# Kernel tuning notes

Hardware: AMD Instinct MI355X
Metric: run time of the kernel (lower is better)

Reference implementation:

```python
import jax, jax.numpy as jnp
import numpy as np

B, N, D = 8, 4096, 1024
NC, NU = 8, 32            # core / universal experts (num_experts=16, occ_factor=1/4)
E = NC + NU               # 40 total experts
S = 2                     # slots per expert
HC, HU = 4 * D, D         # core hidden = 4*dim, occ hidden = 4*occ_factor*dim = dim
L2_EPS = 1e-6
LN_EPS = 1e-5


def l2norm(x):
    n = jnp.sqrt(jnp.sum(x * x, axis=-1, keepdims=True))
    return x * (1.0 / (n + L2_EPS))


def layernorm(x, g, b):
    mu = jnp.mean(x, axis=-1, keepdims=True)
    var = jnp.mean((x - mu) ** 2, axis=-1, keepdims=True)
    return (x - mu) / jnp.sqrt(var + LN_EPS) * g + b


def entmax15(z):
    # exact 1.5-entmax over last axis (sorted algorithm, Peters et al. 2019)
    z = z / 2.0
    z = z - jnp.max(z, axis=-1, keepdims=True)
    zs = -jnp.sort(-z, axis=-1)                      # descending
    K = z.shape[-1]
    k = jnp.arange(1, K + 1, dtype=z.dtype)
    mean = jnp.cumsum(zs, axis=-1) / k
    meansq = jnp.cumsum(zs * zs, axis=-1) / k
    ss = k * (meansq - mean * mean)
    delta = jnp.maximum((1.0 - ss) / k, 1e-12)
    tau = mean - jnp.sqrt(delta)
    support = jnp.sum((tau <= zs).astype(jnp.int32), axis=-1, keepdims=True)
    tau_star = jnp.take_along_axis(tau, support - 1, axis=-1)
    return jnp.maximum(z - tau_star, 0.0) ** 2


def setup_inputs() -> dict:
    key = jax.random.key(0)
    ks = jax.random.split(key, 8)
    return {
        "x": jax.random.normal(ks[0], (B, N, D), jnp.float32),
        "attn_weight": jax.random.uniform(ks[1], (B, 128), jnp.float32),
        "phi": jax.random.normal(ks[2], (E, S, D), jnp.float32) * 0.02,
        "key_gamma": jnp.ones((D,), jnp.float32),
        "key_beta": jnp.zeros((D,), jnp.float32),
        "query_gamma": jnp.ones((D,), jnp.float32),
        "query_beta": jnp.zeros((D,), jnp.float32),
        "ln_gamma": jnp.ones((D,), jnp.float32),
        "ln_beta": jnp.zeros((D,), jnp.float32),
        "scale0": jnp.asarray(0.5, jnp.float32),
        "scale1": jnp.asarray(0.5, jnp.float32),
        "core_w1": jax.random.normal(ks[3], (NC, D, HC), jnp.float32) * (D ** -0.5),
        "core_b1": jnp.zeros((NC, HC), jnp.float32),
        "core_w2": jax.random.normal(ks[4], (NC, HC, D), jnp.float32) * (HC ** -0.5),
        "core_b2": jnp.zeros((NC, D), jnp.float32),
        "occ_w1": jax.random.normal(ks[5], (NU, D, HU), jnp.float32) * (D ** -0.5),
        "occ_b1": jnp.zeros((NU, HU), jnp.float32),
        "occ_w2": jax.random.normal(ks[6], (NU, HU, D), jnp.float32) * (HU ** -0.5),
        "occ_b2": jnp.zeros((NU, D), jnp.float32),
    }


def _expert_mlp(s, w1, b1, w2, b2):
    # s: [b, e, s, d]; per-expert 2-layer MLP with exact GELU
    h = jax.nn.gelu(jnp.einsum('besd,edh->besh', s, w1) + b1[None, :, None, :], approximate=False)
    return jnp.einsum('besh,ehd->besd', h, w2) + b2[None, :, None, :]


def reference(x, attn_weight, phi, key_gamma, key_beta, query_gamma, query_beta,
              ln_gamma, ln_beta, scale0, scale1,
              core_w1, core_b1, core_w2, core_b2,
              occ_w1, occ_b1, occ_w2, occ_b2):
    # keys: OffsetScale then l2norm
    k = l2norm(x * key_gamma + key_beta)
    # queries: OffsetScale -> LayerNorm -> l2norm on phi
    q = layernorm(phi * query_gamma + query_beta, ln_gamma, ln_beta)
    q = l2norm(q)
    logits = jnp.einsum('bnd,esd->bnes', k, q)                      # [B,N,E,S]
    core_mask = (jnp.arange(E) < NC)[None, None, :, None]
    adjusted = jnp.where(core_mask, logits, jnp.asarray(-10000.0, logits.dtype))
    dispatch = jax.nn.softmax(adjusted / scale0, axis=2)            # softmax over experts
    combine = entmax15((adjusted / scale1).reshape(B, N, E * S))    # [B,N,E*S]
    slots = jnp.einsum('bnd,bnes->besd', x, dispatch)               # [B,E,S,D]
    core_out = _expert_mlp(slots[:, :NC], core_w1, core_b1, core_w2, core_b2)
    occ_out = _expert_mlp(slots[:, NC:], occ_w1, occ_b1, occ_w2, occ_b2)
    out = jnp.concatenate([core_out, occ_out], axis=1).reshape(B, E * S, D)
    return jnp.einsum('bsd,bns->bnd', out, combine)                 # [B,N,D]
```

## Files before the change

kernel.cpp:

```cpp
#include <hip/hip_runtime.h>
#include <hip/hip_bf16.h>

#define B_ 8
#define N_ 4096
#define D_ 1024

__global__ __launch_bounds__(64) void k_prep(
    const float* __restrict__ phi, const float* __restrict__ qg, const float* __restrict__ qb,
    const float* __restrict__ lng, const float* __restrict__ lnb,
    const float* __restrict__ kg, const float* __restrict__ kb,
    float* __restrict__ qk, float* __restrict__ cj, float* __restrict__ wbuf)
{
    int r = blockIdx.x;
    int lane = threadIdx.x;
    if (r == 16) {
        float cacc = 0.f;
#pragma unroll
        for (int c = 0; c < 16; ++c) {
            int i = c * 64 + lane;
            float g = kg[i], b = kb[i];
            wbuf[i] = g * g;
            wbuf[1024 + i] = 2.0f * g * b;
            cacc += b * b;
        }
#pragma unroll
        for (int m = 32; m; m >>= 1) cacc += __shfl_xor(cacc, m);
        if (lane == 0) wbuf[2048] = cacc;
        return;
    }
    const float* pr = phi + (size_t)r * D_;
    float v[16];
    float s1 = 0.f;
#pragma unroll
    for (int c = 0; c < 16; ++c) {
        int i = c * 64 + lane;
        v[c] = pr[i] * qg[i] + qb[i];
        s1 += v[c];
    }
#pragma unroll
    for (int m = 32; m; m >>= 1) s1 += __shfl_xor(s1, m);
    float mu = s1 * (1.0f / D_);
    float s2 = 0.f;
#pragma unroll
    for (int c = 0; c < 16; ++c) { float dd = v[c] - mu; s2 += dd * dd; }
#pragma unroll
    for (int m = 32; m; m >>= 1) s2 += __shfl_xor(s2, m);
    float var = s2 * (1.0f / D_);
    float inv = 1.0f / sqrtf(var + 1e-5f);
    float u[16];
    float s3 = 0.f;
#pragma unroll
    for (int c = 0; c < 16; ++c) {
        int i = c * 64 + lane;
        u[c] = (v[c] - mu) * inv * lng[i] + lnb[i];
        s3 += u[c] * u[c];
    }
#pragma unroll
    for (int m = 32; m; m >>= 1) s3 += __shfl_xor(s3, m);
    float rn = 1.0f / (sqrtf(s3) + 1e-6f);
    float cacc = 0.f;
#pragma unroll
    for (int c = 0; c < 16; ++c) {
        int i = c * 64 + lane;
        float qv = u[c] * rn;
        qk[(size_t)r * D_ + i] = qv * kg[i];
        cacc += qv * kb[i];
    }
#pragma unroll
    for (int m = 32; m; m >>= 1) cacc += __shfl_xor(cacc, m);
    if (lane == 0) cj[r] = cacc;
}

__global__ __launch_bounds__(256) void k_logits(
    const float* __restrict__ x, const float* __restrict__ qk,
    const float* __restrict__ wbuf, float* __restrict__ lgbuf)
{
    __shared__ float xs[2][64 * 68];
    __shared__ float qs[2][16 * 64];
    __shared__ float wsd[2][128];

    int tid = threadIdx.x;
    int tok0 = blockIdx.x * 64;
    int tok32 = tid & 31, gg = tid >> 5;
    int sr = tid >> 4, sc = tid & 15;

    float accA[17], accB[17];
#pragma unroll
    for (int v = 0; v < 17; ++v) { accA[v] = 0.f; accB[v] = 0.f; }

    float4 rx[4], rq;
    float rw = 0.f;

    auto STAGE = [&](int dc) {
#pragma unroll
        for (int i = 0; i < 4; ++i)
            rx[i] = *(const float4*)(x + (size_t)(tok0 + sr + 16 * i) * D_ + dc * 64 + sc * 4);
        rq = *(const float4*)(qk + (size_t)sr * D_ + dc * 64 + sc * 4);
        if (tid < 128) rw = wbuf[(size_t)(tid >> 6) * 1024 + dc * 64 + (tid & 63)];
    };
    auto WRITE = [&](int buf) {
#pragma unroll
        for (int i = 0; i < 4; ++i)
            *(float4*)(&xs[buf][(sr + 16 * i) * 68 + sc * 4]) = rx[i];
        ((float4*)qs[buf])[tid] = rq;
        if (tid < 128) wsd[buf][tid] = rw;
    };
    auto COMPUTE = [&](int buf) {
        const float* xpA = &xs[buf][tok32 * 68 + gg * 8];
        const float* xpB = &xs[buf][(32 + tok32) * 68 + gg * 8];
        const float* qp = &qs[buf][gg * 8];
        const float* wp = &wsd[buf][gg * 8];
#pragma unroll
        for (int dl4 = 0; dl4 < 2; ++dl4) {
            float4 xvA = *(const float4*)(xpA + dl4 * 4);
            float4 xvB = *(const float4*)(xpB + dl4 * 4);
            float4 w2v = *(const float4*)(wp + dl4 * 4);
            float4 w1v = *(const float4*)(wp + 64 + dl4 * 4);
            accA[16] += (w2v.x * xvA.x + w1v.x) * xvA.x + (w2v.y * xvA.y + w1v.y) * xvA.y
                      + (w2v.z * xvA.z + w1v.z) * xvA.z + (w2v.w * xvA.w + w1v.w) * xvA.w;
            accB[16] += (w2v.x * xvB.x + w1v.x) * xvB.x + (w2v.y * xvB.y + w1v.y) * xvB.y
                      + (w2v.z * xvB.z + w1v.z) * xvB.z + (w2v.w * xvB.w + w1v.w) * xvB.w;
#pragma unroll
            for (int j = 0; j < 16; ++j) {
                float4 q4 = *(const float4*)(qp + j * 64 + dl4 * 4);
                accA[j] += xvA.x * q4.x + xvA.y * q4.y + xvA.z * q4.z + xvA.w * q4.w;
                accB[j] += xvB.x * q4.x + xvB.y * q4.y + xvB.z * q4.z + xvB.w * q4.w;
            }
        }
    };

    STAGE(0);
    WRITE(0);
    int cur = 0;
#pragma unroll 1
    for (int dc = 0; dc < 16; ++dc) {
        if (dc < 15) STAGE(dc + 1);
        __syncthreads();
        COMPUTE(cur);
        if (dc < 15) WRITE(cur ^ 1);
        cur ^= 1;
    }
    __syncthreads();

    float* red = &xs[0][0];
#pragma unroll
    for (int v = 0; v < 17; ++v) {
        red[(tok32 * 17 + v) * 8 + gg] = accA[v];
        red[((32 + tok32) * 17 + v) * 8 + gg] = accB[v];
    }
    __syncthreads();

#pragma unroll
    for (int it = 0; it < 5; ++it) {
        int idx = tid + it * 256;
        if (idx < 1088) {
            float4 p0 = *(const float4*)(red + idx * 8);
            float4 p1 = *(const float4*)(red + idx * 8 + 4);
            float sum = ((p0.x + p0.y) + (p0.z + p0.w)) + ((p1.x + p1.y) + (p1.z + p1.w));
            int t = idx / 17, v = idx - t * 17;
            lgbuf[(size_t)(tok0 + t) * 20 + v] = sum;
        }
    }
}

__global__ __launch_bounds__(64) void k_epi(
    const float* __restrict__ lgbuf, const float* __restrict__ cj,
    const float* __restrict__ wbuf,
    const float* __restrict__ s0p, const float* __restrict__ s1p,
    float* __restrict__ combine, float* __restrict__ dispatch)
{
    int tok = blockIdx.x * 64 + threadIdx.x;
    const float* lp = lgbuf + (size_t)tok * 20;
    float s[17];
    float4 q0 = *(const float4*)(lp + 0);
    float4 q1 = *(const float4*)(lp + 4);
    float4 q2 = *(const float4*)(lp + 8);
    float4 q3 = *(const float4*)(lp + 12);
    s[0] = q0.x; s[1] = q0.y; s[2] = q0.z; s[3] = q0.w;
    s[4] = q1.x; s[5] = q1.y; s[6] = q1.z; s[7] = q1.w;
    s[8] = q2.x; s[9] = q2.y; s[10] = q2.z; s[11] = q2.w;
    s[12] = q3.x; s[13] = q3.y; s[14] = q3.z; s[15] = q3.w;
    s[16] = lp[16];

    float ss = s[16] + wbuf[2048];
    float rn = 1.0f / (sqrtf(ss) + 1e-6f);
    float inv0 = 1.0f / s0p[0];
    float inv1h = 0.5f / s1p[0];
    float lg[16];
#pragma unroll
    for (int j = 0; j < 16; ++j) lg[j] = (s[j] + cj[j]) * rn;

    float dsp[16];
#pragma unroll
    for (int sl = 0; sl < 2; ++sl) {
        float a[8], m = -1e30f;
#pragma unroll
        for (int ee = 0; ee < 8; ++ee) { a[ee] = lg[2 * ee + sl] * inv0; m = fmaxf(m, a[ee]); }
        float den = 0.f;
#pragma unroll
        for (int ee = 0; ee < 8; ++ee) { a[ee] = expf(a[ee] - m); den += a[ee]; }
        float r = 1.0f / den;
#pragma unroll
        for (int ee = 0; ee < 8; ++ee) dsp[2 * ee + sl] = a[ee] * r;
    }

    float z[16], zmax = -1e30f;
#pragma unroll
    for (int j = 0; j < 16; ++j) { z[j] = lg[j] * inv1h; zmax = fmaxf(zmax, z[j]); }
#pragma unroll
    for (int j = 0; j < 16; ++j) z[j] -= zmax;
    float zsr[16];
#pragma unroll
    for (int j = 0; j < 16; ++j) zsr[j] = z[j];
#pragma unroll
    for (int rr = 0; rr < 16; ++rr) {
#pragma unroll
        for (int jj = (rr & 1); jj + 1 < 16; jj += 2) {
            float aa = zsr[jj], bb = zsr[jj + 1];
            zsr[jj] = fmaxf(aa, bb);
            zsr[jj + 1] = fminf(aa, bb);
        }
    }
    float cs = 0.f, css = 0.f, tau_star = 0.f;
#pragma unroll
    for (int kk = 1; kk <= 16; ++kk) {
        cs += zsr[kk - 1];
        css += zsr[kk - 1] * zsr[kk - 1];
        float fk = (float)kk;
        float mean = cs / fk, msq = css / fk;
        float ssv = fk * (msq - mean * mean);
        float delta = fmaxf((1.0f - ssv) / fk, 1e-12f);
        float tau = mean - sqrtf(delta);
        tau_star = (tau <= zsr[kk - 1]) ? tau : tau_star;
    }
    float4* cw = (float4*)(combine + (size_t)tok * 16);
    float4* dw = (float4*)(dispatch + (size_t)tok * 16);
#pragma unroll
    for (int q4i = 0; q4i < 4; ++q4i) {
        float4 cv, dv;
        float t0 = fmaxf(z[q4i * 4 + 0] - tau_star, 0.f);
        float t1 = fmaxf(z[q4i * 4 + 1] - tau_star, 0.f);
        float t2 = fmaxf(z[q4i * 4 + 2] - tau_star, 0.f);
        float t3 = fmaxf(z[q4i * 4 + 3] - tau_star, 0.f);
        cv.x = t0 * t0; cv.y = t1 * t1; cv.z = t2 * t2; cv.w = t3 * t3;
        dv.x = dsp[q4i * 4 + 0]; dv.y = dsp[q4i * 4 + 1];
        dv.z = dsp[q4i * 4 + 2]; dv.w = dsp[q4i * 4 + 3];
        cw[q4i] = cv;
        dw[q4i] = dv;
    }
}

__global__ __launch_bounds__(256) void k_slots_partial(
    const float* __restrict__ x, const float* __restrict__ dispatch,
    float* __restrict__ partial)
{
    __shared__ float sm[1024];
    int nc = blockIdx.x, b = blockIdx.y;
    int tid = threadIdx.x;
    int n0 = nc * 64;
    ((float4*)sm)[tid] = ((const float4*)(dispatch + ((size_t)b * N_ + n0) * 16))[tid];
    __syncthreads();

    const float* xp = x + ((size_t)b * N_ + n0) * D_ + tid * 4;
    float4 acc[16];
#pragma unroll
    for (int j = 0; j < 16; ++j) { acc[j].x = 0.f; acc[j].y = 0.f; acc[j].z = 0.f; acc[j].w = 0.f; }
#pragma unroll 8
    for (int n = 0; n < 64; ++n) {
        float4 xv = *(const float4*)(xp + (size_t)n * D_);
        const float4* q4 = (const float4*)(sm + n * 16);
        float4 s0 = q4[0], s1 = q4[1], s2 = q4[2], s3 = q4[3];
        acc[0].x  += s0.x * xv.x; acc[0].y  += s0.x * xv.y; acc[0].z  += s0.x * xv.z; acc[0].w  += s0.x * xv.w;
        acc[1].x  += s0.y * xv.x; acc[1].y  += s0.y * xv.y; acc[1].z  += s0.y * xv.z; acc[1].w  += s0.y * xv.w;
        acc[2].x  += s0.z * xv.x; acc[2].y  += s0.z * xv.y; acc[2].z  += s0.z * xv.z; acc[2].w  += s0.z * xv.w;
        acc[3].x  += s0.w * xv.x; acc[3].y  += s0.w * xv.y; acc[3].z  += s0.w * xv.z; acc[3].w  += s0.w * xv.w;
        acc[4].x  += s1.x * xv.x; acc[4].y  += s1.x * xv.y; acc[4].z  += s1.x * xv.z; acc[4].w  += s1.x * xv.w;
        acc[5].x  += s1.y * xv.x; acc[5].y  += s1.y * xv.y; acc[5].z  += s1.y * xv.z; acc[5].w  += s1.y * xv.w;
        acc[6].x  += s1.z * xv.x; acc[6].y  += s1.z * xv.y; acc[6].z  += s1.z * xv.z; acc[6].w  += s1.z * xv.w;
        acc[7].x  += s1.w * xv.x; acc[7].y  += s1.w * xv.y; acc[7].z  += s1.w * xv.z; acc[7].w  += s1.w * xv.w;
        acc[8].x  += s2.x * xv.x; acc[8].y  += s2.x * xv.y; acc[8].z  += s2.x * xv.z; acc[8].w  += s2.x * xv.w;
        acc[9].x  += s2.y * xv.x; acc[9].y  += s2.y * xv.y; acc[9].z  += s2.y * xv.z; acc[9].w  += s2.y * xv.w;
        acc[10].x += s2.z * xv.x; acc[10].y += s2.z * xv.y; acc[10].z += s2.z * xv.z; acc[10].w += s2.z * xv.w;
        acc[11].x += s2.w * xv.x; acc[11].y += s2.w * xv.y; acc[11].z += s2.w * xv.z; acc[11].w += s2.w * xv.w;
        acc[12].x += s3.x * xv.x; acc[12].y += s3.x * xv.y; acc[12].z += s3.x * xv.z; acc[12].w += s3.x * xv.w;
        acc[13].x += s3.y * xv.x; acc[13].y += s3.y * xv.y; acc[13].z += s3.y * xv.z; acc[13].w += s3.y * xv.w;
        acc[14].x += s3.z * xv.x; acc[14].y += s3.z * xv.y; acc[14].z += s3.z * xv.z; acc[14].w += s3.z * xv.w;
        acc[15].x += s3.w * xv.x; acc[15].y += s3.w * xv.y; acc[15].z += s3.w * xv.z; acc[15].w += s3.w * xv.w;
    }
    float* op = partial + (((size_t)b * 64 + nc) * 16) * 1024 + tid * 4;
#pragma unroll
    for (int j = 0; j < 16; ++j)
        *(float4*)(op + (size_t)j * 1024) = acc[j];
}

__global__ __launch_bounds__(256) void k_slots_reduce(
    const float* __restrict__ partial, float* __restrict__ slotsT)
{
    int j = blockIdx.x, b = blockIdx.y;
    int tid = threadIdx.x;
    const float* p = partial + ((size_t)(b * 64) * 16 + j) * 1024 + tid * 4;
    float4 s; s.x = 0.f; s.y = 0.f; s.z = 0.f; s.w = 0.f;
#pragma unroll 8
    for (int nc = 0; nc < 64; ++nc) {
        float4 v = *(const float4*)(p + (size_t)nc * 16384);
        s.x += v.x; s.y += v.y; s.z += v.z; s.w += v.w;
    }
    int e = j >> 1, sl = j & 1;
    int t = b * 2 + sl;
    float* o = slotsT + ((size_t)e * 1024 + tid * 4) * 16 + t;
    o[0] = s.x; o[16] = s.y; o[32] = s.z; o[48] = s.w;
}

__global__ __launch_bounds__(256) void k_mlp1(
    const float* __restrict__ w1, const float* __restrict__ slotsT,
    float* __restrict__ p1)
{
    __shared__ float sm[1024];
    int cc = blockIdx.x, ks = blockIdx.y, e = blockIdx.z;
    int tid = threadIdx.x;
    int k0 = ks * 64;
    int col = cc * 1024 + tid * 4;
    ((float4*)sm)[tid] = ((const float4*)(slotsT + ((size_t)e * 1024 + k0) * 16))[tid];
    __syncthreads();

    const float* wp = w1 + (size_t)e * 1024 * 4096 + (size_t)k0 * 4096 + col;
    float4 acc[16];
#pragma unroll
    for (int t = 0; t < 16; ++t) { acc[t].x = 0.f; acc[t].y = 0.f; acc[t].z = 0.f; acc[t].w = 0.f; }
#pragma unroll 8
    for (int kk = 0; kk < 64; ++kk) {
        float4 w = *(const float4*)(wp + (size_t)kk * 4096);
        const float4* q4 = (const float4*)(sm + kk * 16);
        float4 s0 = q4[0], s1 = q4[1], s2 = q4[2], s3 = q4[3];
        acc[0].x  += s0.x * w.x; acc[0].y  += s0.x * w.y; acc[0].z  += s0.x * w.z; acc[0].w  += s0.x * w.w;
        acc[1].x  += s0.y * w.x; acc[1].y  += s0.y * w.y; acc[1].z  += s0.y * w.z; acc[1].w  += s0.y * w.w;
        acc[2].x  += s0.z * w.x; acc[2].y  += s0.z * w.y; acc[2].z  += s0.z * w.z; acc[2].w  += s0.z * w.w;
        acc[3].x  += s0.w * w.x; acc[3].y  += s0.w * w.y; acc[3].z  += s0.w * w.z; acc[3].w  += s0.w * w.w;
        acc[4].x  += s1.x * w.x; acc[4].y  += s1.x * w.y; acc[4].z  += s1.x * w.z; acc[4].w  += s1.x * w.w;
        acc[5].x  += s1.y * w.x; acc[5].y  += s1.y * w.y; acc[5].z  += s1.y * w.z; acc[5].w  += s1.y * w.w;
        acc[6].x  += s1.z * w.x; acc[6].y  += s1.z * w.y; acc[6].z  += s1.z * w.z; acc[6].w  += s1.z * w.w;
        acc[7].x  += s1.w * w.x; acc[7].y  += s1.w * w.y; acc[7].z  += s1.w * w.z; acc[7].w  += s1.w * w.w;
        acc[8].x  += s2.x * w.x; acc[8].y  += s2.x * w.y; acc[8].z  += s2.x * w.z; acc[8].w  += s2.x * w.w;
        acc[9].x  += s2.y * w.x; acc[9].y  += s2.y * w.y; acc[9].z  += s2.y * w.z; acc[9].w  += s2.y * w.w;
        acc[10].x += s2.z * w.x; acc[10].y += s2.z * w.y; acc[10].z += s2.z * w.z; acc[10].w += s2.z * w.w;
        acc[11].x += s2.w * w.x; acc[11].y += s2.w * w.y; acc[11].z += s2.w * w.z; acc[11].w += s2.w * w.w;
        acc[12].x += s3.x * w.x; acc[12].y += s3.x * w.y; acc[12].z += s3.x * w.z; acc[12].w += s3.x * w.w;
        acc[13].x += s3.y * w.x; acc[13].y += s3.y * w.y; acc[13].z += s3.y * w.z; acc[13].w += s3.y * w.w;
        acc[14].x += s3.z * w.x; acc[14].y += s3.z * w.y; acc[14].z += s3.z * w.z; acc[14].w += s3.z * w.w;
        acc[15].x += s3.w * w.x; acc[15].y += s3.w * w.y; acc[15].z += s3.w * w.z; acc[15].w += s3.w * w.w;
    }
    float av0[16], av1[16], av2[16], av3[16];
#pragma unroll
    for (int t = 0; t < 16; ++t) { av0[t] = acc[t].x; av1[t] = acc[t].y; av2[t] = acc[t].z; av3[t] = acc[t].w; }
    float* op = p1 + (((size_t)ks * 8 + e) * 4096 + col) * 16;
#pragma unroll
    for (int q = 0; q < 4; ++q) {
        *(float4*)(op + 0 * 16 + q * 4) = make_float4(av0[q*4+0], av0[q*4+1], av0[q*4+2], av0[q*4+3]);
        *(float4*)(op + 1 * 16 + q * 4) = make_float4(av1[q*4+0], av1[q*4+1], av1[q*4+2], av1[q*4+3]);
        *(float4*)(op + 2 * 16 + q * 4) = make_float4(av2[q*4+0], av2[q*4+1], av2[q*4+2], av2[q*4+3]);
        *(float4*)(op + 3 * 16 + q * 4) = make_float4(av3[q*4+0], av3[q*4+1], av3[q*4+2], av3[q*4+3]);
    }
}

__global__ __launch_bounds__(256) void k_red1(
    const float* __restrict__ p1, const float* __restrict__ b1,
    float* __restrict__ hT)
{
    int idx = blockIdx.x * 256 + threadIdx.x;
    int q = idx & 3, col = (idx >> 2) & 4095, e = idx >> 14;
    const float* p = p1 + ((size_t)e * 4096 + col) * 16 + q * 4;
    float4 s; s.x = 0.f; s.y = 0.f; s.z = 0.f; s.w = 0.f;
#pragma unroll
    for (int ks = 0; ks < 16; ++ks) {
        float4 v = *(const float4*)(p + (size_t)ks * 524288);
        s.x += v.x; s.y += v.y; s.z += v.z; s.w += v.w;
    }
    float bb = b1[(size_t)e * 4096 + col];
    s.x += bb; s.y += bb; s.z += bb; s.w += bb;
    s.x = 0.5f * s.x * (1.0f + erff(s.x * 0.70710678118654752f));
    s.y = 0.5f * s.y * (1.0f + erff(s.y * 0.70710678118654752f));
    s.z = 0.5f * s.z * (1.0f + erff(s.z * 0.70710678118654752f));
    s.w = 0.5f * s.w * (1.0f + erff(s.w * 0.70710678118654752f));
    *(float4*)(hT + ((size_t)e * 4096 + col) * 16 + q * 4) = s;
}

__global__ __launch_bounds__(256) void k_mlp2(
    const float* __restrict__ w2, const float* __restrict__ hT,
    float* __restrict__ p2)
{
    __shared__ float sm[1024];
    int ks = blockIdx.x, e = blockIdx.y;
    int tid = threadIdx.x;
    int k0 = ks * 64;
    int col = tid * 4;
    ((float4*)sm)[tid] = ((const float4*)(hT + ((size_t)e * 4096 + k0) * 16))[tid];
    __syncthreads();

    const float* wp = w2 + (size_t)e * 4096 * 1024 + (size_t)k0 * 1024 + col;
    float4 acc[16];
#pragma unroll
    for (int t = 0; t < 16; ++t) { acc[t].x = 0.f; acc[t].y = 0.f; acc[t].z = 0.f; acc[t].w = 0.f; }
#pragma unroll 8
    for (int kk = 0; kk < 64; ++kk) {
        float4 w = *(const float4*)(wp + (size_t)kk * 1024);
        const float4* q4 = (const float4*)(sm + kk * 16);
        float4 s0 = q4[0], s1 = q4[1], s2 = q4[2], s3 = q4[3];
        acc[0].x  += s0.x * w.x; acc[0].y  += s0.x * w.y; acc[0].z  += s0.x * w.z; acc[0].w  += s0.x * w.w;
        acc[1].x  += s0.y * w.x; acc[1].y  += s0.y * w.y; acc[1].z  += s0.y * w.z; acc[1].w  += s0.y * w.w;
        acc[2].x  += s0.z * w.x; acc[2].y  += s0.z * w.y; acc[2].z  += s0.z * w.z; acc[2].w  += s0.z * w.w;
        acc[3].x  += s0.w * w.x; acc[3].y  += s0.w * w.y; acc[3].z  += s0.w * w.z; acc[3].w  += s0.w * w.w;
        acc[4].x  += s1.x * w.x; acc[4].y  += s1.x * w.y; acc[4].z  += s1.x * w.z; acc[4].w  += s1.x * w.w;
        acc[5].x  += s1.y * w.x; acc[5].y  += s1.y * w.y; acc[5].z  += s1.y * w.z; acc[5].w  += s1.y * w.w;
        acc[6].x  += s1.z * w.x; acc[6].y  += s1.z * w.y; acc[6].z  += s1.z * w.z; acc[6].w  += s1.z * w.w;
        acc[7].x  += s1.w * w.x; acc[7].y  += s1.w * w.y; acc[7].z  += s1.w * w.z; acc[7].w  += s1.w * w.w;
        acc[8].x  += s2.x * w.x; acc[8].y  += s2.x * w.y; acc[8].z  += s2.x * w.z; acc[8].w  += s2.x * w.w;
        acc[9].x  += s2.y * w.x; acc[9].y  += s2.y * w.y; acc[9].z  += s2.y * w.z; acc[9].w  += s2.y * w.w;
        acc[10].x += s2.z * w.x; acc[10].y += s2.z * w.y; acc[10].z += s2.z * w.z; acc[10].w += s2.z * w.w;
        acc[11].x += s2.w * w.x; acc[11].y += s2.w * w.y; acc[11].z += s2.w * w.z; acc[11].w += s2.w * w.w;
        acc[12].x += s3.x * w.x; acc[12].y += s3.x * w.y; acc[12].z += s3.x * w.z; acc[12].w += s3.x * w.w;
        acc[13].x += s3.y * w.x; acc[13].y += s3.y * w.y; acc[13].z += s3.y * w.z; acc[13].w += s3.y * w.w;
        acc[14].x += s3.z * w.x; acc[14].y += s3.z * w.y; acc[14].z += s3.z * w.z; acc[14].w += s3.z * w.w;
        acc[15].x += s3.w * w.x; acc[15].y += s3.w * w.y; acc[15].z += s3.w * w.z; acc[15].w += s3.w * w.w;
    }
    float av0[16], av1[16], av2[16], av3[16];
#pragma unroll
    for (int t = 0; t < 16; ++t) { av0[t] = acc[t].x; av1[t] = acc[t].y; av2[t] = acc[t].z; av3[t] = acc[t].w; }
    float* op = p2 + (((size_t)ks * 8 + e) * 1024 + col) * 16;
#pragma unroll
    for (int q = 0; q < 4; ++q) {
        *(float4*)(op + 0 * 16 + q * 4) = make_float4(av0[q*4+0], av0[q*4+1], av0[q*4+2], av0[q*4+3]);
        *(float4*)(op + 1 * 16 + q * 4) = make_float4(av1[q*4+0], av1[q*4+1], av1[q*4+2], av1[q*4+3]);
        *(float4*)(op + 2 * 16 + q * 4) = make_float4(av2[q*4+0], av2[q*4+1], av2[q*4+2], av2[q*4+3]);
        *(float4*)(op + 3 * 16 + q * 4) = make_float4(av3[q*4+0], av3[q*4+1], av3[q*4+2], av3[q*4+3]);
    }
}

__global__ __launch_bounds__(256) void k_red2(
    const float* __restrict__ p2, const float* __restrict__ b2,
    float* __restrict__ co)
{
    int idx = blockIdx.x * 256 + threadIdx.x;
    int q = idx & 3, d = (idx >> 2) & 1023, e = idx >> 12;
    const float* p = p2 + ((size_t)e * 1024 + d) * 16 + q * 4;
    float4 s; s.x = 0.f; s.y = 0.f; s.z = 0.f; s.w = 0.f;
#pragma unroll 8
    for (int ks = 0; ks < 64; ++ks) {
        float4 v = *(const float4*)(p + (size_t)ks * 131072);
        s.x += v.x; s.y += v.y; s.z += v.z; s.w += v.w;
    }
    float bb = b2[(size_t)e * 1024 + d];
    float vv[4] = { s.x + bb, s.y + bb, s.z + bb, s.w + bb };
#pragma unroll
    for (int u = 0; u < 4; ++u) {
        int t = q * 4 + u;
        int b = t >> 1, sl = t & 1;
        co[((size_t)b * 16 + e * 2 + sl) * 1024 + d] = vv[u];
    }
}

__global__ __launch_bounds__(256) void k_out(
    const float* __restrict__ co, const float* __restrict__ combine,
    float* __restrict__ out)
{
    __shared__ float sm[1024];
    int b = blockIdx.y, tile = blockIdx.x;
    int tid = threadIdx.x;
    ((float4*)sm)[tid] = ((const float4*)(combine + ((size_t)b * N_ + tile * 64) * 16))[tid];
    float4 cv[16];
#pragma unroll
    for (int j = 0; j < 16; ++j)
        cv[j] = ((const float4*)(co + ((size_t)b * 16 + j) * 1024))[tid];
    __syncthreads();
    float4* ob = (float4*)(out + ((size_t)b * N_ + tile * 64) * 1024) + tid;
#pragma unroll 2
    for (int it = 0; it < 64; ++it) {
        const float* cm = sm + it * 16;
        float4 acc; acc.x = 0.f; acc.y = 0.f; acc.z = 0.f; acc.w = 0.f;
#pragma unroll
        for (int j = 0; j < 16; ++j) {
            float wj = cm[j];
            acc.x += wj * cv[j].x; acc.y += wj * cv[j].y;
            acc.z += wj * cv[j].z; acc.w += wj * cv[j].w;
        }
        ob[(size_t)it * 256] = acc;
    }
}

extern "C" void kernel_launch(void* const* d_in, const int* in_sizes, int n_in,
                              void* d_out, int out_size, void* d_ws, size_t ws_size,
                              hipStream_t stream)
{
    const float* x   = (const float*)d_in[0];
    const float* phi = (const float*)d_in[2];
    const float* kg  = (const float*)d_in[3];
    const float* kb  = (const float*)d_in[4];
    const float* qg  = (const float*)d_in[5];
    const float* qb  = (const float*)d_in[6];
    const float* lng = (const float*)d_in[7];
    const float* lnb = (const float*)d_in[8];
    const float* s0  = (const float*)d_in[9];
    const float* s1  = (const float*)d_in[10];
    const float* w1  = (const float*)d_in[11];
    const float* b1  = (const float*)d_in[12];
    const float* w2  = (const float*)d_in[13];
    const float* b2  = (const float*)d_in[14];

    float* out = (float*)d_out;
    float* ws  = (float*)d_ws;

    float* qk       = ws;
    float* cj       = qk + 16384;
    float* wbuf     = cj + 16;
    float* combine  = wbuf + 2064;
    float* dispatch = combine + 524288;
    float* slotsT   = dispatch + 524288;
    float* hT       = slotsT + 131072;
    float* co       = hT + 524288;
    float* arena    = co + 131072;
    float* lgbuf    = arena;
    float* spart    = arena;
    float* p1       = arena;
    float* p2       = arena;

    k_prep         <<<dim3(17),        dim3(64),  0, stream>>>(phi, qg, qb, lng, lnb, kg, kb, qk, cj, wbuf);
    k_logits       <<<dim3(512),       dim3(256), 0, stream>>>(x, qk, wbuf, lgbuf);
    k_epi          <<<dim3(512),       dim3(64),  0, stream>>>(lgbuf, cj, wbuf, s0, s1, combine, dispatch);
    k_slots_partial<<<dim3(64, 8),     dim3(256), 0, stream>>>(x, dispatch, spart);
    k_slots_reduce <<<dim3(16, 8),     dim3(256), 0, stream>>>(spart, slotsT);
    k_mlp1         <<<dim3(4, 16, 8),  dim3(256), 0, stream>>>(w1, slotsT, p1);
    k_red1         <<<dim3(512),       dim3(256), 0, stream>>>(p1, b1, hT);
    k_mlp2         <<<dim3(64, 8),     dim3(256), 0, stream>>>(w2, hT, p2);
    k_red2         <<<dim3(128),       dim3(256), 0, stream>>>(p2, b2, co);
    k_out          <<<dim3(64, 8),     dim3(256), 0, stream>>>(co, combine, out);
}
```

Before: 248.9 us.

## Fuse hidden-layer reduction+GELU into second MLP, enlarge tiles for logits and slots

The separate k_red1 kernel is removed. The split-K reduction of the first expert MLP, plus bias and GELU, now runs inside the second MLP kernel's shared-memory staging, and the intermediate hT buffer is dropped. K-split chunks for slots, MLP1 and MLP2 grow from 64 to 128, which halves the partial buffers and the reduce work. The logits kernel now handles 128 tokens per block with single-buffered shared memory and more accumulators per thread. This trades fewer launches and less partial traffic for fewer blocks (lower parallelism), higher register pressure, and the loss of double buffering in k_logits.

```diff
diff --git a/kernel.cpp b/kernel.cpp
--- a/kernel.cpp
+++ b/kernel.cpp
@@ -75,90 +75,104 @@
     const float* __restrict__ x, const float* __restrict__ qk,
     const float* __restrict__ wbuf, float* __restrict__ lgbuf)
 {
-    __shared__ float xs[2][64 * 68];
-    __shared__ float qs[2][16 * 64];
-    __shared__ float wsd[2][128];
+    __shared__ float xs[128 * 68];
+    __shared__ float qs[16 * 64];
+    __shared__ float wsd[128];
 
     int tid = threadIdx.x;
-    int tok0 = blockIdx.x * 64;
+    int tok0 = blockIdx.x * 128;
     int tok32 = tid & 31, gg = tid >> 5;
     int sr = tid >> 4, sc = tid & 15;
 
-    float accA[17], accB[17];
-#pragma unroll
-    for (int v = 0; v < 17; ++v) { accA[v] = 0.f; accB[v] = 0.f; }
-
-    float4 rx[4], rq;
+    float acc[4][17];
+#pragma unroll
+    for (int t4 = 0; t4 < 4; ++t4)
+#pragma unroll
+        for (int v = 0; v < 17; ++v) acc[t4][v] = 0.f;
+
+    float4 rx[8], rq;
     float rw = 0.f;
 
     auto STAGE = [&](int dc) {
 #pragma unroll
-        for (int i = 0; i < 4; ++i)
+        for (int i = 0; i < 8; ++i)
             rx[i] = *(const float4*)(x + (size_t)(tok0 + sr + 16 * i) * D_ + dc * 64 + sc * 4);
         rq = *(const float4*)(qk + (size_t)sr * D_ + dc * 64 + sc * 4);
         if (tid < 128) rw = wbuf[(size_t)(tid >> 6) * 1024 + dc * 64 + (tid & 63)];
     };
-    auto WRITE = [&](int buf) {
-#pragma unroll
-        for (int i = 0; i < 4; ++i)
-            *(float4*)(&xs[buf][(sr + 16 * i) * 68 + sc * 4]) = rx[i];
-        ((float4*)qs[buf])[tid] = rq;
-        if (tid < 128) wsd[buf][tid] = rw;
+    auto WRITE = [&]() {
+#pragma unroll
+        for (int i = 0; i < 8; ++i)
+            *(float4*)(&xs[(sr + 16 * i) * 68 + sc * 4]) = rx[i];
+        ((float4*)qs)[tid] = rq;
+        if (tid < 128) wsd[tid] = rw;
     };
-    auto COMPUTE = [&](int buf) {
-        const float* xpA = &xs[buf][tok32 * 68 + gg * 8];
-        const float* xpB = &xs[buf][(32 + tok32) * 68 + gg * 8];
-        const float* qp = &qs[buf][gg * 8];
-        const float* wp = &wsd[buf][gg * 8];
+    auto COMPUTE = [&]() {
+        const float* wp = &wsd[gg * 8];
+        const float* qp = &qs[gg * 8];
 #pragma unroll
         for (int dl4 = 0; dl4 < 2; ++dl4) {
-            float4 xvA = *(const float4*)(xpA + dl4 * 4);
-            float4 xvB = *(const float4*)(xpB + dl4 * 4);
+            float4 xv0 = *(const float4*)(&xs[(0 * 32 + tok32) * 68 + gg * 8 + dl4 * 4]);
+            float4 xv1 = *(const float4*)(&xs[(1 * 32 + tok32) * 68 + gg * 8 + dl4 * 4]);
+            float4 xv2 = *(const float4*)(&xs[(2 * 32 + tok32) * 68 + gg * 8 + dl4 * 4]);
+            float4 xv3 = *(const float4*)(&xs[(3 * 32 + tok32) * 68 + gg * 8 + dl4 * 4]);
             float4 w2v = *(const float4*)(wp + dl4 * 4);
             float4 w1v = *(const float4*)(wp + 64 + dl4 * 4);
-            accA[16] += (w2v.x * xvA.x + w1v.x) * xvA.x + (w2v.y * xvA.y + w1v.y) * xvA.y
-                      + (w2v.z * xvA.z + w1v.z) * xvA.z + (w2v.w * xvA.w + w1v.w) * xvA.w;
-            accB[16] += (w2v.x * xvB.x + w1v.x) * xvB.x + (w2v.y * xvB.y + w1v.y) * xvB.y
-                      + (w2v.z * xvB.z + w1v.z) * xvB.z + (w2v.w * xvB.w + w1v.w) * xvB.w;
+            acc[0][16] += (w2v.x * xv0.x + w1v.x) * xv0.x + (w2v.y * xv0.y + w1v.y) * xv0.y
+                        + (w2v.z * xv0.z + w1v.z) * xv0.z + (w2v.w * xv0.w + w1v.w) * xv0.w;
+            acc[1][16] += (w2v.x * xv1.x + w1v.x) * xv1.x + (w2v.y * xv1.y + w1v.y) * xv1.y
+                        + (w2v.z * xv1.z + w1v.z) * xv1.z + (w2v.w * xv1.w + w1v.w) * xv1.w;
+            acc[2][16] += (w2v.x * xv2.x + w1v.x) * xv2.x + (w2v.y * xv2.y + w1v.y) * xv2.y
+                        + (w2v.z * xv2.z + w1v.z) * xv2.z + (w2v.w * xv2.w + w1v.w) * xv2.w;
+            acc[3][16] += (w2v.x * xv3.x + w1v.x) * xv3.x + (w2v.y * xv3.y + w1v.y) * xv3.y
+                        + (w2v.z * xv3.z + w1v.z) * xv3.z + (w2v.w * xv3.w + w1v.w) * xv3.w;
 #pragma unroll
             for (int j = 0; j < 16; ++j) {
                 float4 q4 = *(const float4*)(qp + j * 64 + dl4 * 4);
-                accA[j] += xvA.x * q4.x + xvA.y * q4.y + xvA.z * q4.z + xvA.w * q4.w;
-                accB[j] += xvB.x * q4.x + xvB.y * q4.y + xvB.z * q4.z + xvB.w * q4.w;
+                acc[0][j] += xv0.x * q4.x + xv0.y * q4.y + xv0.z * q4.z + xv0.w * q4.w;
+                acc[1][j] += xv1.x * q4.x + xv1.y * q4.y + xv1.z * q4.z + xv1.w * q4.w;
+                acc[2][j] += xv2.x * q4.x + xv2.y * q4.y + xv2.z * q4.z + xv2.w * q4.w;
+                acc[3][j] += xv3.x * q4.x + xv3.y * q4.y + xv3.z * q4.z + xv3.w * q4.w;
             }
         }
     };
 
     STAGE(0);
-    WRITE(0);
-    int cur = 0;
+    WRITE();
+    __syncthreads();
 #pragma unroll 1
     for (int dc = 0; dc < 16; ++dc) {
         if (dc < 15) STAGE(dc + 1);
+        COMPUTE();
+        if (dc < 15) {
+            __syncthreads();
+            WRITE();
+            __syncthreads();
+        }
+    }
+
+    float* red = xs;
+#pragma unroll
+    for (int half = 0; half < 2; ++half) {
         __syncthreads();
-        COMPUTE(cur);
-        if (dc < 15) WRITE(cur ^ 1);
-        cur ^= 1;
-    }
-    __syncthreads();
-
-    float* red = &xs[0][0];
-#pragma unroll
-    for (int v = 0; v < 17; ++v) {
-        red[(tok32 * 17 + v) * 8 + gg] = accA[v];
-        red[((32 + tok32) * 17 + v) * 8 + gg] = accB[v];
-    }
-    __syncthreads();
-
-#pragma unroll
-    for (int it = 0; it < 5; ++it) {
-        int idx = tid + it * 256;
-        if (idx < 1088) {
-            float4 p0 = *(const float4*)(red + idx * 8);
-            float4 p1 = *(const float4*)(red + idx * 8 + 4);
-            float sum = ((p0.x + p0.y) + (p0.z + p0.w)) + ((p1.x + p1.y) + (p1.z + p1.w));
-            int t = idx / 17, v = idx - t * 17;
-            lgbuf[(size_t)(tok0 + t) * 20 + v] = sum;
+#pragma unroll
+        for (int u = 0; u < 2; ++u) {
+            int t4 = 2 * half + u;
+            int r = u * 32 + tok32;
+#pragma unroll
+            for (int v = 0; v < 17; ++v) red[(r * 17 + v) * 8 + gg] = acc[t4][v];
+        }
+        __syncthreads();
+#pragma unroll
+        for (int it = 0; it < 5; ++it) {
+            int idx = tid + it * 256;
+            if (idx < 1088) {
+                float4 p0 = *(const float4*)(red + idx * 8);
+                float4 p1v = *(const float4*)(red + idx * 8 + 4);
+                float sum = ((p0.x + p0.y) + (p0.z + p0.w)) + ((p1v.x + p1v.y) + (p1v.z + p1v.w));
+                int t = idx / 17, v = idx - t * 17;
+                lgbuf[(size_t)(tok0 + half * 64 + t) * 20 + v] = sum;
+            }
         }
     }
 }
@@ -252,13 +266,15 @@
 
 __global__ __launch_bounds__(256) void k_slots_partial(
     const float* __restrict__ x, const float* __restrict__ dispatch,
-    float* __restrict__ partial)
-{
-    __shared__ float sm[1024];
+    float* __restrict__ spart)
+{
+    __shared__ float sm[2048];
     int nc = blockIdx.x, b = blockIdx.y;
     int tid = threadIdx.x;
-    int n0 = nc * 64;
-    ((float4*)sm)[tid] = ((const float4*)(dispatch + ((size_t)b * N_ + n0) * 16))[tid];
+    int n0 = nc * 128;
+    const float4* src = (const float4*)(dispatch + ((size_t)b * N_ + n0) * 16);
+    ((float4*)sm)[tid] = src[tid];
+    ((float4*)sm)[tid + 256] = src[tid + 256];
     __syncthreads();
 
     const float* xp = x + ((size_t)b * N_ + n0) * D_ + tid * 4;
@@ -266,7 +282,7 @@
 #pragma unroll
     for (int j = 0; j < 16; ++j) { acc[j].x = 0.f; acc[j].y = 0.f; acc[j].z = 0.f; acc[j].w = 0.f; }
 #pragma unroll 8
-    for (int n = 0; n < 64; ++n) {
+    for (int n = 0; n < 128; ++n) {
         float4 xv = *(const float4*)(xp + (size_t)n * D_);
         const float4* q4 = (const float4*)(sm + n * 16);
         float4 s0 = q4[0], s1 = q4[1], s2 = q4[2], s3 = q4[3];
@@ -287,21 +303,21 @@
         acc[14].x += s3.z * xv.x; acc[14].y += s3.z * xv.y; acc[14].z += s3.z * xv.z; acc[14].w += s3.z * xv.w;
         acc[15].x += s3.w * xv.x; acc[15].y += s3.w * xv.y; acc[15].z += s3.w * xv.z; acc[15].w += s3.w * xv.w;
     }
-    float* op = partial + (((size_t)b * 64 + nc) * 16) * 1024 + tid * 4;
+    float* op = spart + (((size_t)b * 32 + nc) * 16) * 1024 + tid * 4;
 #pragma unroll
     for (int j = 0; j < 16; ++j)
         *(float4*)(op + (size_t)j * 1024) = acc[j];
 }
 
 __global__ __launch_bounds__(256) void k_slots_reduce(
-    const float* __restrict__ partial, float* __restrict__ slotsT)
+    const float* __restrict__ spart, float* __restrict__ slotsT)
 {
     int j = blockIdx.x, b = blockIdx.y;
     int tid = threadIdx.x;
-    const float* p = partial + ((size_t)(b * 64) * 16 + j) * 1024 + tid * 4;
+    const float* p = spart + ((size_t)(b * 32) * 16 + j) * 1024 + tid * 4;
     float4 s; s.x = 0.f; s.y = 0.f; s.z = 0.f; s.w = 0.f;
 #pragma unroll 8
-    for (int nc = 0; nc < 64; ++nc) {
+    for (int nc = 0; nc < 32; ++nc) {
         float4 v = *(const float4*)(p + (size_t)nc * 16384);
         s.x += v.x; s.y += v.y; s.z += v.z; s.w += v.w;
     }
@@ -315,12 +331,14 @@
     const float* __restrict__ w1, const float* __restrict__ slotsT,
     float* __restrict__ p1)
 {
-    __shared__ float sm[1024];
+    __shared__ float sm[2048];
     int cc = blockIdx.x, ks = blockIdx.y, e = blockIdx.z;
     int tid = threadIdx.x;
-    int k0 = ks * 64;
+    int k0 = ks * 128;
     int col = cc * 1024 + tid * 4;
-    ((float4*)sm)[tid] = ((const float4*)(slotsT + ((size_t)e * 1024 + k0) * 16))[tid];
+    const float4* src = (const float4*)(slotsT + ((size_t)e * 1024 + k0) * 16);
+    ((float4*)sm)[tid] = src[tid];
+    ((float4*)sm)[tid + 256] = src[tid + 256];
     __syncthreads();
 
     const float* wp = w1 + (size_t)e * 1024 * 4096 + (size_t)k0 * 4096 + col;
@@ -328,7 +346,7 @@
 #pragma unroll
     for (int t = 0; t < 16; ++t) { acc[t].x = 0.f; acc[t].y = 0.f; acc[t].z = 0.f; acc[t].w = 0.f; }
 #pragma unroll 8
-    for (int kk = 0; kk < 64; ++kk) {
+    for (int kk = 0; kk < 128; ++kk) {
         float4 w = *(const float4*)(wp + (size_t)kk * 4096);
         const float4* q4 = (const float4*)(sm + kk * 16);
         float4 s0 = q4[0], s1 = q4[1], s2 = q4[2], s3 = q4[3];
@@ -362,38 +380,35 @@
     }
 }
 
-__global__ __launch_bounds__(256) void k_red1(
-    const float* __restrict__ p1, const float* __restrict__ b1,
-    float* __restrict__ hT)
-{
-    int idx = blockIdx.x * 256 + threadIdx.x;
-    int q = idx & 3, col = (idx >> 2) & 4095, e = idx >> 14;
-    const float* p = p1 + ((size_t)e * 4096 + col) * 16 + q * 4;
-    float4 s; s.x = 0.f; s.y = 0.f; s.z = 0.f; s.w = 0.f;
-#pragma unroll
-    for (int ks = 0; ks < 16; ++ks) {
-        float4 v = *(const float4*)(p + (size_t)ks * 524288);
-        s.x += v.x; s.y += v.y; s.z += v.z; s.w += v.w;
-    }
-    float bb = b1[(size_t)e * 4096 + col];
-    s.x += bb; s.y += bb; s.z += bb; s.w += bb;
-    s.x = 0.5f * s.x * (1.0f + erff(s.x * 0.70710678118654752f));
-    s.y = 0.5f * s.y * (1.0f + erff(s.y * 0.70710678118654752f));
-    s.z = 0.5f * s.z * (1.0f + erff(s.z * 0.70710678118654752f));
-    s.w = 0.5f * s.w * (1.0f + erff(s.w * 0.70710678118654752f));
-    *(float4*)(hT + ((size_t)e * 4096 + col) * 16 + q * 4) = s;
-}
-
-__global__ __launch_bounds__(256) void k_mlp2(
-    const float* __restrict__ w2, const float* __restrict__ hT,
-    float* __restrict__ p2)
-{
-    __shared__ float sm[1024];
+__global__ __launch_bounds__(256) void k_mlp2f(
+    const float* __restrict__ w2, const float* __restrict__ p1,
+    const float* __restrict__ b1, float* __restrict__ p2)
+{
+    __shared__ float sm[2048];
     int ks = blockIdx.x, e = blockIdx.y;
     int tid = threadIdx.x;
-    int k0 = ks * 64;
+    int k0 = ks * 128;
     int col = tid * 4;
-    ((float4*)sm)[tid] = ((const float4*)(hT + ((size_t)e * 4096 + k0) * 16))[tid];
+
+#pragma unroll
+    for (int i = 0; i < 2; ++i) {
+        int fidx = tid * 2 + i;
+        const float* pp = p1 + (size_t)e * 65536 + (size_t)k0 * 16 + fidx * 4;
+        float4 s; s.x = 0.f; s.y = 0.f; s.z = 0.f; s.w = 0.f;
+#pragma unroll
+        for (int ksp = 0; ksp < 8; ++ksp) {
+            float4 v = *(const float4*)(pp + (size_t)ksp * 524288);
+            s.x += v.x; s.y += v.y; s.z += v.z; s.w += v.w;
+        }
+        int colh = k0 + fidx / 4;
+        float bb = b1[(size_t)e * 4096 + colh];
+        s.x += bb; s.y += bb; s.z += bb; s.w += bb;
+        s.x = 0.5f * s.x * (1.0f + erff(s.x * 0.70710678118654752f));
+        s.y = 0.5f * s.y * (1.0f + erff(s.y * 0.70710678118654752f));
+        s.z = 0.5f * s.z * (1.0f + erff(s.z * 0.70710678118654752f));
+        s.w = 0.5f * s.w * (1.0f + erff(s.w * 0.70710678118654752f));
+        *(float4*)(&sm[fidx * 4]) = s;
+    }
     __syncthreads();
 
     const float* wp = w2 + (size_t)e * 4096 * 1024 + (size_t)k0 * 1024 + col;
@@ -401,7 +416,7 @@
 #pragma unroll
     for (int t = 0; t < 16; ++t) { acc[t].x = 0.f; acc[t].y = 0.f; acc[t].z = 0.f; acc[t].w = 0.f; }
 #pragma unroll 8
-    for (int kk = 0; kk < 64; ++kk) {
+    for (int kk = 0; kk < 128; ++kk) {
         float4 w = *(const float4*)(wp + (size_t)kk * 1024);
         const float4* q4 = (const float4*)(sm + kk * 16);
         float4 s0 = q4[0], s1 = q4[1], s2 = q4[2], s3 = q4[3];
@@ -444,7 +459,7 @@
     const float* p = p2 + ((size_t)e * 1024 + d) * 16 + q * 4;
     float4 s; s.x = 0.f; s.y = 0.f; s.z = 0.f; s.w = 0.f;
 #pragma unroll 8
-    for (int ks = 0; ks < 64; ++ks) {
+    for (int ks = 0; ks < 32; ++ks) {
         float4 v = *(const float4*)(p + (size_t)ks * 131072);
         s.x += v.x; s.y += v.y; s.z += v.z; s.w += v.w;
     }
@@ -514,22 +529,21 @@
     float* combine  = wbuf + 2064;
     float* dispatch = combine + 524288;
     float* slotsT   = dispatch + 524288;
-    float* hT       = slotsT + 131072;
-    float* co       = hT + 524288;
-    float* arena    = co + 131072;
-    float* lgbuf    = arena;
-    float* spart    = arena;
-    float* p1       = arena;
-    float* p2       = arena;
-
-    k_prep         <<<dim3(17),        dim3(64),  0, stream>>>(phi, qg, qb, lng, lnb, kg, kb, qk, cj, wbuf);
-    k_logits       <<<dim3(512),       dim3(256), 0, stream>>>(x, qk, wbuf, lgbuf);
-    k_epi          <<<dim3(512),       dim3(64),  0, stream>>>(lgbuf, cj, wbuf, s0, s1, combine, dispatch);
-    k_slots_partial<<<dim3(64, 8),     dim3(256), 0, stream>>>(x, dispatch, spart);
-    k_slots_reduce <<<dim3(16, 8),     dim3(256), 0, stream>>>(spart, slotsT);
-    k_mlp1         <<<dim3(4, 16, 8),  dim3(256), 0, stream>>>(w1, slotsT, p1);
-    k_red1         <<<dim3(512),       dim3(256), 0, stream>>>(p1, b1, hT);
-    k_mlp2         <<<dim3(64, 8),     dim3(256), 0, stream>>>(w2, hT, p2);
-    k_red2         <<<dim3(128),       dim3(256), 0, stream>>>(p2, b2, co);
-    k_out          <<<dim3(64, 8),     dim3(256), 0, stream>>>(co, combine, out);
-}
+    float* co       = slotsT + 131072;
+    float* arenaA   = co + 131072;
+    float* arenaB   = arenaA + 4194304;
+    float* lgbuf    = arenaA;
+    float* spart    = arenaA;
+    float* p1       = arenaA;
+    float* p2       = arenaB;
+
+    k_prep         <<<dim3(17),       dim3(64),  0, stream>>>(phi, qg, qb, lng, lnb, kg, kb, qk, cj, wbuf);
+    k_logits       <<<dim3(256),      dim3(256), 0, stream>>>(x, qk, wbuf, lgbuf);
+    k_epi          <<<dim3(512),      dim3(64),  0, stream>>>(lgbuf, cj, wbuf, s0, s1, combine, dispatch);
+    k_slots_partial<<<dim3(32, 8),    dim3(256), 0, stream>>>(x, dispatch, spart);
+    k_slots_reduce <<<dim3(16, 8),    dim3(256), 0, stream>>>(spart, slotsT);
+    k_mlp1         <<<dim3(4, 8, 8),  dim3(256), 0, stream>>>(w1, slotsT, p1);
+    k_mlp2f        <<<dim3(32, 8),    dim3(256), 0, stream>>>(w2, p1, b1, p2);
+    k_red2         <<<dim3(128),      dim3(256), 0, stream>>>(p2, b2, co);
+    k_out          <<<dim3(64, 8),    dim3(256), 0, stream>>>(co, combine, out);
+}
```

Result: slower. 308.2 us (+23.8%).
